# Optimization experiments

Hardware: AMD Instinct MI355X
Metric: run time of the kernel (lower is better)

Reference implementation:

```python
import jax, jax.numpy as jnp
import numpy as np

D_MODEL = 1024
N_HEADS = 16
D_K = D_MODEL // N_HEADS


def setup_inputs() -> dict:
    key = jax.random.key(0)
    kx, kq, kk, kv, ko = jax.random.split(key, 5)
    s = 1.0 / np.sqrt(D_MODEL)
    return {
        "x": jax.random.normal(kx, (4, 2048, D_MODEL), dtype=jnp.float32),
        "W_q": jax.random.normal(kq, (D_MODEL, D_MODEL), dtype=jnp.float32) * s,
        "W_k": jax.random.normal(kk, (D_MODEL, D_MODEL), dtype=jnp.float32) * s,
        "W_v": jax.random.normal(kv, (D_MODEL, D_MODEL), dtype=jnp.float32) * s,
        "W_o": jax.random.normal(ko, (D_MODEL, D_MODEL), dtype=jnp.float32) * s,
    }


def reference(x, W_q, W_k, W_v, W_o):
    B, S, _ = x.shape
    # torch nn.Linear computes x @ W.T; our W_* stored as [out, in]-equivalent square,
    # use plain x @ W (equivalent parameterization for a random weight).
    def split_heads(t):  # [B,S,D] -> [B,H,S,d_k]
        return t.reshape(B, S, N_HEADS, D_K).transpose(0, 2, 1, 3)

    Q = split_heads(x @ W_q)
    K = split_heads(x @ W_k)
    V = split_heads(x @ W_v)
    scale = 1.0 / np.sqrt(D_K).astype(np.float32)
    scores = jnp.einsum('bhqd,bhkd->bhqk', Q, K) * scale  # [B,H,S,S]
    causal_mask = jnp.tril(jnp.ones((S, S), dtype=bool))  # True = keep
    scores = jnp.where(causal_mask, scores, jnp.float32(-jnp.inf))
    attn = jax.nn.softmax(scores, axis=-1)
    out = jnp.einsum('bhqk,bhkd->bhqd', attn, V)  # [B,H,S,d_k]
    out = out.transpose(0, 2, 1, 3).reshape(B, S, D_MODEL)
    return out @ W_o
```

## Files before the change

kernel.cpp:

```cpp
#include <hip/hip_runtime.h>
#include <hip/hip_bf16.h>
#include <stdint.h>

#define B_SZ 4
#define SEQ 2048
#define DM 1024
#define NH 16
#define DK 64
#define BH (B_SZ * NH)
#define M_TOT (B_SZ * SEQ)

typedef unsigned short u16;
typedef u16 u16x8 __attribute__((ext_vector_type(8)));
typedef __bf16 bf16x8 __attribute__((ext_vector_type(8)));
typedef float f32x4 __attribute__((ext_vector_type(4)));

__device__ __forceinline__ u16 f2bf(float f) {
    union { float f; uint32_t u; } v; v.f = f;
    uint32_t u = v.u;
    return (u16)((u + 0x7FFFu + ((u >> 16) & 1u)) >> 16);
}

__device__ __forceinline__ u16 f2bf_trunc(float f) {
    union { float f; uint32_t u; } v; v.f = f;
    return (u16)(v.u >> 16);
}

__device__ __forceinline__ f32x4 mfma16(u16x8 a, u16x8 b, f32x4 c) {
    return __builtin_amdgcn_mfma_f32_16x16x32_bf16(
        __builtin_bit_cast(bf16x8, a), __builtin_bit_cast(bf16x8, b), c, 0, 0, 0);
}

__device__ __forceinline__ void gload16_lds(const void* g, void* l) {
    __builtin_amdgcn_global_load_lds(
        (const __attribute__((address_space(1))) void*)(uintptr_t)g,
        (__attribute__((address_space(3))) void*)(uintptr_t)l, 16, 0, 0);
}

__global__ void cvt_bf16_kernel(const float* __restrict__ in, u16* __restrict__ out, int n4) {
    int i = blockIdx.x * blockDim.x + threadIdx.x;
    if (i < n4) {
        float4 v = ((const float4*)in)[i];
        ushort4 o;
        o.x = f2bf(v.x); o.y = f2bf(v.y); o.z = f2bf(v.z); o.w = f2bf(v.w);
        ((ushort4*)out)[i] = o;
    }
}

__global__ void transpose_w_kernel(const float* __restrict__ W0, const float* __restrict__ W1,
                                   u16* __restrict__ Wt) {
    __shared__ u16 tile[32][33];
    int bx = blockIdx.x, by = blockIdx.y, z = blockIdx.z;
    const float* W = z ? W1 : W0;
    u16* Wd = Wt + (size_t)z * DM * DM;
    int t = threadIdx.x;
    for (int i = 0; i < 4; i++) {
        int idx = t + i * 256;
        int r = idx >> 5, c = idx & 31;
        tile[r][c] = f2bf(W[(by * 32 + r) * DM + bx * 32 + c]);
    }
    __syncthreads();
    for (int i = 0; i < 4; i++) {
        int idx = t + i * 256;
        int r2 = idx >> 5, c2 = idx & 31;
        Wd[(bx * 32 + r2) * DM + by * 32 + c2] = tile[c2][r2];
    }
}

__global__ void vtrans_kernel(const u16* __restrict__ V, u16* __restrict__ Vt) {
    __shared__ u16 t[64][66];
    int s0 = blockIdx.x * 64, bh = blockIdx.y;
    int tid = threadIdx.x, lane = tid & 63, wave = tid >> 6;
    const u16* Vg = V + (size_t)bh * SEQ * DK;
    u16* Og = Vt + (size_t)bh * DK * SEQ;
    for (int i = 0; i < 2; i++) {
        int s = lane;
        int dc = wave + 4 * i;
        u16x8 v = *(const u16x8*)(&Vg[(size_t)(s0 + s) * DK + dc * 8]);
        for (int j = 0; j < 8; j++) t[dc * 8 + j][s] = v[j];
    }
    __syncthreads();
    int d = tid >> 2, ch = tid & 3;
    u16 tmp[16];
    for (int j = 0; j < 16; j++) tmp[j] = t[d][ch * 16 + j];
    *(uint4*)(&Og[(size_t)d * SEQ + s0 + ch * 16]) = *(uint4*)(&tmp[0]);
    *(uint4*)(&Og[(size_t)d * SEQ + s0 + ch * 16 + 8]) = *(uint4*)(&tmp[8]);
}

template <int AFP32, int MODE>
__global__ __launch_bounds__(256, 2) void gemm128(
    const void* __restrict__ Ain, const u16* __restrict__ Bt,
    void* __restrict__ C0p, void* __restrict__ C1p, float scale0) {
    __shared__ u16 As[128][32];
    __shared__ u16 Bs[128][32];
    const int K = DM;
    int m0 = blockIdx.x * 128;
    int n0 = blockIdx.y * 128;
    int tid = threadIdx.x;
    int lane = tid & 63, wave = tid >> 6;
    int quad = lane >> 4, l15 = lane & 15;
    int wm = wave >> 1, wn = wave & 1;

    f32x4 acc[4][4];
    for (int i = 0; i < 4; i++)
        for (int j = 0; j < 4; j++) acc[i][j] = f32x4{0.f, 0.f, 0.f, 0.f};

    int rS = lane >> 2;
    int cS = (lane & 3) * 8;

    for (int k0 = 0; k0 < K; k0 += 32) {
        __syncthreads();
        if (AFP32) {
            const float* A = (const float*)Ain;
            for (int i = 0; i < 4; i++) {
                int idx = tid + i * 256;
                int r = idx >> 3, c = (idx & 7) * 4;
                float4 v = *(const float4*)(&A[(size_t)(m0 + r) * K + k0 + c]);
                ushort4 o;
                o.x = f2bf(v.x); o.y = f2bf(v.y); o.z = f2bf(v.z); o.w = f2bf(v.w);
                *(ushort4*)(&As[r][c]) = o;
            }
        } else {
            const u16* A = (const u16*)Ain;
            const u16* ga = &A[(size_t)(m0 + wave * 32 + rS) * K + k0 + cS];
            gload16_lds(ga, &As[wave * 32][0]);
            gload16_lds(ga + (size_t)16 * K, &As[wave * 32 + 16][0]);
        }
        {
            const u16* gb = &Bt[(size_t)(n0 + wave * 32 + rS) * K + k0 + cS];
            gload16_lds(gb, &Bs[wave * 32][0]);
            gload16_lds(gb + (size_t)16 * K, &Bs[wave * 32 + 16][0]);
        }
        __syncthreads();
        u16x8 af[4], bfv[4];
        for (int mt = 0; mt < 4; mt++)
            af[mt] = *(const u16x8*)(&As[wm * 64 + mt * 16 + l15][quad * 8]);
        for (int nt = 0; nt < 4; nt++)
            bfv[nt] = *(const u16x8*)(&Bs[wn * 64 + nt * 16 + l15][quad * 8]);
        for (int mt = 0; mt < 4; mt++)
            for (int nt = 0; nt < 4; nt++)
                acc[mt][nt] = mfma16(af[mt], bfv[nt], acc[mt][nt]);
    }

    for (int mt = 0; mt < 4; mt++)
        for (int nt = 0; nt < 4; nt++)
            for (int r = 0; r < 4; r++) {
                int m = m0 + wm * 64 + mt * 16 + quad * 4 + r;
                int n = n0 + wn * 64 + nt * 16 + l15;
                float v = acc[mt][nt][r];
                if (MODE == 0) {
                    v *= (n < 1024) ? scale0 : 1.0f;
                    u16* C = (n < 1024) ? (u16*)C0p : (u16*)C1p;
                    int ne = n & 1023;
                    int b = m >> 11, s = m & 2047;
                    int h = ne >> 6, d = ne & 63;
                    C[(((size_t)(b * NH + h) * SEQ) + s) * DK + d] = f2bf(v);
                } else {
                    ((float*)C0p)[(size_t)m * DM + n] = v;
                }
            }
}

__global__ __launch_bounds__(256, 4) void attn_kernel(
    const u16* __restrict__ Qb, const u16* __restrict__ Kb,
    const u16* __restrict__ Vtb, u16* __restrict__ AOb) {
    __shared__ u16 Kl[2][64][32];
    __shared__ u16 Vl[2][64][32];
    __shared__ u16 Pl[64][72];

    int bh = blockIdx.x;
    int p = blockIdx.y;
    int tid = threadIdx.x, lane = tid & 63, wave = tid >> 6;
    int quad = lane >> 4, l15 = lane & 15;
    int b = bh >> 4, h = bh & 15;

    const u16* Qg = Qb + (size_t)bh * SEQ * DK;
    const u16* Kg = Kb + (size_t)bh * SEQ * DK;
    const u16* Vg = Vtb + (size_t)bh * DK * SEQ;

    int rS = lane >> 2;
    int cS = (lane & 3) * 8;
    u16* Pw = &Pl[wave * 16][0];

    for (int ph = 0; ph < 2; ph++) {
        int qs = ph ? (31 - p) : p;
        int q0 = qs * 64;

        u16x8 aq[2];
        for (int kc = 0; kc < 2; kc++)
            aq[kc] = *(const u16x8*)(
                &Qg[(size_t)(q0 + wave * 16 + l15) * DK + kc * 32 + quad * 8]);

        float lsum[4];
        f32x4 O[4];
        for (int r = 0; r < 4; r++) lsum[r] = 0.f;
        for (int nt = 0; nt < 4; nt++) O[nt] = f32x4{0.f, 0.f, 0.f, 0.f};

        for (int kt = 0; kt <= qs; kt++) {
            int k0 = kt * 64;
            __syncthreads();
            {
                const u16* gk = &Kg[(size_t)(k0 + wave * 16 + rS) * DK + cS];
                gload16_lds(gk, &Kl[0][wave * 16][0]);
                gload16_lds(gk + 32, &Kl[1][wave * 16][0]);
                const u16* gv = &Vg[(size_t)(wave * 16 + rS) * SEQ + k0 + cS];
                gload16_lds(gv, &Vl[0][wave * 16][0]);
                gload16_lds(gv + 32, &Vl[1][wave * 16][0]);
            }
            __syncthreads();

            f32x4 sc[4];
            for (int nt = 0; nt < 4; nt++) {
                u16x8 b0 = *(const u16x8*)(&Kl[0][nt * 16 + l15][quad * 8]);
                u16x8 b1 = *(const u16x8*)(&Kl[1][nt * 16 + l15][quad * 8]);
                f32x4 z = f32x4{0.f, 0.f, 0.f, 0.f};
                z = mfma16(aq[0], b0, z);
                z = mfma16(aq[1], b1, z);
                sc[nt] = z;
            }
            if (kt == qs) {
                for (int nt = 0; nt < 4; nt++)
                    for (int r = 0; r < 4; r++) {
                        int qq = wave * 16 + quad * 4 + r;
                        int kk = nt * 16 + l15;
                        float e = exp2f(sc[nt][r]);
                        float pv = (kk <= qq) ? e : 0.f;
                        sc[nt][r] = pv;
                        lsum[r] += pv;
                    }
            } else {
                for (int nt = 0; nt < 4; nt++)
                    for (int r = 0; r < 4; r++) {
                        float pv = exp2f(sc[nt][r]);
                        sc[nt][r] = pv;
                        lsum[r] += pv;
                    }
            }
            for (int nt = 0; nt < 4; nt++)
                for (int r = 0; r < 4; r++)
                    Pw[(size_t)(quad * 4 + r) * 72 + nt * 16 + l15] = f2bf_trunc(sc[nt][r]);
            u16x8 ap0 = *(const u16x8*)(&Pw[(size_t)l15 * 72 + quad * 8]);
            u16x8 ap1 = *(const u16x8*)(&Pw[(size_t)l15 * 72 + 32 + quad * 8]);
            for (int nt = 0; nt < 4; nt++) {
                u16x8 b0 = *(const u16x8*)(&Vl[0][nt * 16 + l15][quad * 8]);
                u16x8 b1 = *(const u16x8*)(&Vl[1][nt * 16 + l15][quad * 8]);
                O[nt] = mfma16(ap0, b0, O[nt]);
                O[nt] = mfma16(ap1, b1, O[nt]);
            }
        }

        for (int r = 0; r < 4; r++) {
            float s = lsum[r];
            for (int off = 1; off < 16; off <<= 1) s += __shfl_xor(s, off, 64);
            float inv = 1.0f / s;
            int q = q0 + wave * 16 + quad * 4 + r;
            for (int nt = 0; nt < 4; nt++) {
                int d = nt * 16 + l15;
                AOb[((size_t)(b * SEQ + q)) * DM + h * DK + d] = f2bf(O[nt][r] * inv);
            }
        }
    }
}

extern "C" void kernel_launch(void* const* d_in, const int* in_sizes, int n_in,
                              void* d_out, int out_size, void* d_ws, size_t ws_size,
                              hipStream_t stream) {
    const float* x = (const float*)d_in[0];
    const float* Wq = (const float*)d_in[1];
    const float* Wk = (const float*)d_in[2];
    const float* Wv = (const float*)d_in[3];
    const float* Wo = (const float*)d_in[4];

    const size_t HALF = (size_t)M_TOT * DM * 2;
    char* S0 = (char*)d_ws;
    char* S1 = (char*)d_ws + HALF;
    char* D0 = (char*)d_out;
    char* D1 = (char*)d_out + HALF;

    u16* xb   = (u16*)S0;
    u16* Qb   = (u16*)S1;
    u16* Kb   = (u16*)D1;
    u16* Vb   = (u16*)D0;
    u16* Vt   = (u16*)S0;
    u16* AOb  = (u16*)D0;
    u16* wqk  = (u16*)D0;
    u16* wvt  = (u16*)S0;
    u16* wot  = (u16*)D1;
    float* Cf = (float*)d_ws;

    const float cscale = 0.125f * 1.44269504088896f;
    dim3 tg2(32, 32, 2);
    dim3 tg1(32, 32, 1);

    int n4 = M_TOT * DM / 4;
    cvt_bf16_kernel<<<n4 / 256, 256, 0, stream>>>(x, xb, n4);

    transpose_w_kernel<<<tg2, 256, 0, stream>>>(Wq, Wk, wqk);
    dim3 gqk(M_TOT / 128, 2048 / 128);
    gemm128<0, 0><<<gqk, 256, 0, stream>>>(xb, wqk, (void*)Qb, (void*)Kb, cscale);

    transpose_w_kernel<<<tg1, 256, 0, stream>>>(Wv, Wv, wvt);
    dim3 gg(M_TOT / 128, DM / 128);
    gemm128<1, 0><<<gg, 256, 0, stream>>>(x, wvt, (void*)Vb, (void*)Vb, 1.0f);

    dim3 vg(SEQ / 64, BH);
    vtrans_kernel<<<vg, 256, 0, stream>>>(Vb, Vt);

    dim3 ag(BH, 16);
    attn_kernel<<<ag, 256, 0, stream>>>(Qb, Kb, Vt, AOb);

    transpose_w_kernel<<<tg1, 256, 0, stream>>>(Wo, Wo, wot);
    gemm128<0, 1><<<gg, 256, 0, stream>>>(AOb, wot, (void*)Cf, (void*)Cf, 1.0f);

    hipMemcpyAsync(d_out, d_ws, 2 * HALF, hipMemcpyDeviceToDevice, stream);
}
```

Baseline: 296.8 us.

## Fuse V transpose into GEMM epilogue, split attention blocks, drop final memcpy

The V projection GEMM gets a new epilogue mode that writes the bf16 transposed V layout directly, which removes the separate transpose kernel and its read/write pass. The attention kernel no longer pairs a short and a long query tile per block. It launches one block per query tile with heaviest-first ordering and raises the occupancy hint to 6. The output projection now writes straight into the output buffer, so the final device-to-device memcpy is gone and buffer aliasing is rearranged. Risks are uncoalesced strided stores in the transposed epilogue and load imbalance without the paired tiles.

```diff
diff --git a/kernel.cpp b/kernel.cpp
--- a/kernel.cpp
+++ b/kernel.cpp
@@ -65,26 +65,6 @@
         int r2 = idx >> 5, c2 = idx & 31;
         Wd[(bx * 32 + r2) * DM + by * 32 + c2] = tile[c2][r2];
     }
-}
-
-__global__ void vtrans_kernel(const u16* __restrict__ V, u16* __restrict__ Vt) {
-    __shared__ u16 t[64][66];
-    int s0 = blockIdx.x * 64, bh = blockIdx.y;
-    int tid = threadIdx.x, lane = tid & 63, wave = tid >> 6;
-    const u16* Vg = V + (size_t)bh * SEQ * DK;
-    u16* Og = Vt + (size_t)bh * DK * SEQ;
-    for (int i = 0; i < 2; i++) {
-        int s = lane;
-        int dc = wave + 4 * i;
-        u16x8 v = *(const u16x8*)(&Vg[(size_t)(s0 + s) * DK + dc * 8]);
-        for (int j = 0; j < 8; j++) t[dc * 8 + j][s] = v[j];
-    }
-    __syncthreads();
-    int d = tid >> 2, ch = tid & 3;
-    u16 tmp[16];
-    for (int j = 0; j < 16; j++) tmp[j] = t[d][ch * 16 + j];
-    *(uint4*)(&Og[(size_t)d * SEQ + s0 + ch * 16]) = *(uint4*)(&tmp[0]);
-    *(uint4*)(&Og[(size_t)d * SEQ + s0 + ch * 16 + 8]) = *(uint4*)(&tmp[8]);
 }
 
 template <int AFP32, int MODE>
@@ -155,21 +135,26 @@
                     int b = m >> 11, s = m & 2047;
                     int h = ne >> 6, d = ne & 63;
                     C[(((size_t)(b * NH + h) * SEQ) + s) * DK + d] = f2bf(v);
+                } else if (MODE == 1) {
+                    ((float*)C0p)[(size_t)m * DM + n] = v;
                 } else {
-                    ((float*)C0p)[(size_t)m * DM + n] = v;
+                    int b = m >> 11, s = m & 2047;
+                    int h = n >> 6, d = n & 63;
+                    ((u16*)C0p)[(((size_t)(b * NH + h) * DK) + d) * SEQ + s] = f2bf(v);
                 }
             }
 }
 
-__global__ __launch_bounds__(256, 4) void attn_kernel(
+__global__ __launch_bounds__(256, 6) void attn_kernel(
     const u16* __restrict__ Qb, const u16* __restrict__ Kb,
     const u16* __restrict__ Vtb, u16* __restrict__ AOb) {
     __shared__ u16 Kl[2][64][32];
     __shared__ u16 Vl[2][64][32];
-    __shared__ u16 Pl[64][72];
+    __shared__ u16 Pl[64][68];
 
     int bh = blockIdx.x;
-    int p = blockIdx.y;
+    int qs = 31 - blockIdx.y;
+    int q0 = qs * 64;
     int tid = threadIdx.x, lane = tid & 63, wave = tid >> 6;
     int quad = lane >> 4, l15 = lane & 15;
     int b = bh >> 4, h = bh & 15;
@@ -182,82 +167,77 @@
     int cS = (lane & 3) * 8;
     u16* Pw = &Pl[wave * 16][0];
 
-    for (int ph = 0; ph < 2; ph++) {
-        int qs = ph ? (31 - p) : p;
-        int q0 = qs * 64;
-
-        u16x8 aq[2];
-        for (int kc = 0; kc < 2; kc++)
-            aq[kc] = *(const u16x8*)(
-                &Qg[(size_t)(q0 + wave * 16 + l15) * DK + kc * 32 + quad * 8]);
-
-        float lsum[4];
-        f32x4 O[4];
-        for (int r = 0; r < 4; r++) lsum[r] = 0.f;
-        for (int nt = 0; nt < 4; nt++) O[nt] = f32x4{0.f, 0.f, 0.f, 0.f};
-
-        for (int kt = 0; kt <= qs; kt++) {
-            int k0 = kt * 64;
-            __syncthreads();
-            {
-                const u16* gk = &Kg[(size_t)(k0 + wave * 16 + rS) * DK + cS];
-                gload16_lds(gk, &Kl[0][wave * 16][0]);
-                gload16_lds(gk + 32, &Kl[1][wave * 16][0]);
-                const u16* gv = &Vg[(size_t)(wave * 16 + rS) * SEQ + k0 + cS];
-                gload16_lds(gv, &Vl[0][wave * 16][0]);
-                gload16_lds(gv + 32, &Vl[1][wave * 16][0]);
-            }
-            __syncthreads();
-
-            f32x4 sc[4];
-            for (int nt = 0; nt < 4; nt++) {
-                u16x8 b0 = *(const u16x8*)(&Kl[0][nt * 16 + l15][quad * 8]);
-                u16x8 b1 = *(const u16x8*)(&Kl[1][nt * 16 + l15][quad * 8]);
-                f32x4 z = f32x4{0.f, 0.f, 0.f, 0.f};
-                z = mfma16(aq[0], b0, z);
-                z = mfma16(aq[1], b1, z);
-                sc[nt] = z;
-            }
-            if (kt == qs) {
-                for (int nt = 0; nt < 4; nt++)
-                    for (int r = 0; r < 4; r++) {
-                        int qq = wave * 16 + quad * 4 + r;
-                        int kk = nt * 16 + l15;
-                        float e = exp2f(sc[nt][r]);
-                        float pv = (kk <= qq) ? e : 0.f;
-                        sc[nt][r] = pv;
-                        lsum[r] += pv;
-                    }
-            } else {
-                for (int nt = 0; nt < 4; nt++)
-                    for (int r = 0; r < 4; r++) {
-                        float pv = exp2f(sc[nt][r]);
-                        sc[nt][r] = pv;
-                        lsum[r] += pv;
-                    }
-            }
+    u16x8 aq[2];
+    for (int kc = 0; kc < 2; kc++)
+        aq[kc] = *(const u16x8*)(
+            &Qg[(size_t)(q0 + wave * 16 + l15) * DK + kc * 32 + quad * 8]);
+
+    float lsum[4];
+    f32x4 O[4];
+    for (int r = 0; r < 4; r++) lsum[r] = 0.f;
+    for (int nt = 0; nt < 4; nt++) O[nt] = f32x4{0.f, 0.f, 0.f, 0.f};
+
+    for (int kt = 0; kt <= qs; kt++) {
+        int k0 = kt * 64;
+        __syncthreads();
+        {
+            const u16* gk = &Kg[(size_t)(k0 + wave * 16 + rS) * DK + cS];
+            gload16_lds(gk, &Kl[0][wave * 16][0]);
+            gload16_lds(gk + 32, &Kl[1][wave * 16][0]);
+            const u16* gv = &Vg[(size_t)(wave * 16 + rS) * SEQ + k0 + cS];
+            gload16_lds(gv, &Vl[0][wave * 16][0]);
+            gload16_lds(gv + 32, &Vl[1][wave * 16][0]);
+        }
+        __syncthreads();
+
+        f32x4 sc[4];
+        for (int nt = 0; nt < 4; nt++) {
+            u16x8 b0 = *(const u16x8*)(&Kl[0][nt * 16 + l15][quad * 8]);
+            u16x8 b1 = *(const u16x8*)(&Kl[1][nt * 16 + l15][quad * 8]);
+            f32x4 z = f32x4{0.f, 0.f, 0.f, 0.f};
+            z = mfma16(aq[0], b0, z);
+            z = mfma16(aq[1], b1, z);
+            sc[nt] = z;
+        }
+        if (kt == qs) {
             for (int nt = 0; nt < 4; nt++)
-                for (int r = 0; r < 4; r++)
-                    Pw[(size_t)(quad * 4 + r) * 72 + nt * 16 + l15] = f2bf_trunc(sc[nt][r]);
-            u16x8 ap0 = *(const u16x8*)(&Pw[(size_t)l15 * 72 + quad * 8]);
-            u16x8 ap1 = *(const u16x8*)(&Pw[(size_t)l15 * 72 + 32 + quad * 8]);
-            for (int nt = 0; nt < 4; nt++) {
-                u16x8 b0 = *(const u16x8*)(&Vl[0][nt * 16 + l15][quad * 8]);
-                u16x8 b1 = *(const u16x8*)(&Vl[1][nt * 16 + l15][quad * 8]);
-                O[nt] = mfma16(ap0, b0, O[nt]);
-                O[nt] = mfma16(ap1, b1, O[nt]);
-            }
-        }
-
-        for (int r = 0; r < 4; r++) {
-            float s = lsum[r];
-            for (int off = 1; off < 16; off <<= 1) s += __shfl_xor(s, off, 64);
-            float inv = 1.0f / s;
-            int q = q0 + wave * 16 + quad * 4 + r;
-            for (int nt = 0; nt < 4; nt++) {
-                int d = nt * 16 + l15;
-                AOb[((size_t)(b * SEQ + q)) * DM + h * DK + d] = f2bf(O[nt][r] * inv);
-            }
+                for (int r = 0; r < 4; r++) {
+                    int qq = wave * 16 + quad * 4 + r;
+                    int kk = nt * 16 + l15;
+                    float e = exp2f(sc[nt][r]);
+                    float pv = (kk <= qq) ? e : 0.f;
+                    sc[nt][r] = pv;
+                    lsum[r] += pv;
+                }
+        } else {
+            for (int nt = 0; nt < 4; nt++)
+                for (int r = 0; r < 4; r++) {
+                    float pv = exp2f(sc[nt][r]);
+                    sc[nt][r] = pv;
+                    lsum[r] += pv;
+                }
+        }
+        for (int nt = 0; nt < 4; nt++)
+            for (int r = 0; r < 4; r++)
+                Pw[(size_t)(quad * 4 + r) * 68 + nt * 16 + l15] = f2bf_trunc(sc[nt][r]);
+        u16x8 ap0 = *(const u16x8*)(&Pw[(size_t)l15 * 68 + quad * 8]);
+        u16x8 ap1 = *(const u16x8*)(&Pw[(size_t)l15 * 68 + 32 + quad * 8]);
+        for (int nt = 0; nt < 4; nt++) {
+            u16x8 b0 = *(const u16x8*)(&Vl[0][nt * 16 + l15][quad * 8]);
+            u16x8 b1 = *(const u16x8*)(&Vl[1][nt * 16 + l15][quad * 8]);
+            O[nt] = mfma16(ap0, b0, O[nt]);
+            O[nt] = mfma16(ap1, b1, O[nt]);
+        }
+    }
+
+    for (int r = 0; r < 4; r++) {
+        float s = lsum[r];
+        for (int off = 1; off < 16; off <<= 1) s += __shfl_xor(s, off, 64);
+        float inv = 1.0f / s;
+        int q = q0 + wave * 16 + quad * 4 + r;
+        for (int nt = 0; nt < 4; nt++) {
+            int d = nt * 16 + l15;
+            AOb[((size_t)(b * SEQ + q)) * DM + h * DK + d] = f2bf(O[nt][r] * inv);
         }
     }
 }
@@ -270,6 +250,7 @@
     const float* Wk = (const float*)d_in[2];
     const float* Wv = (const float*)d_in[3];
     const float* Wo = (const float*)d_in[4];
+    float* out = (float*)d_out;
 
     const size_t HALF = (size_t)M_TOT * DM * 2;
     char* S0 = (char*)d_ws;
@@ -277,20 +258,19 @@
     char* D0 = (char*)d_out;
     char* D1 = (char*)d_out + HALF;
 
-    u16* xb   = (u16*)S0;
-    u16* Qb   = (u16*)S1;
-    u16* Kb   = (u16*)D1;
-    u16* Vb   = (u16*)D0;
-    u16* Vt   = (u16*)S0;
-    u16* AOb  = (u16*)D0;
-    u16* wqk  = (u16*)D0;
-    u16* wvt  = (u16*)S0;
-    u16* wot  = (u16*)D1;
-    float* Cf = (float*)d_ws;
+    u16* xb  = (u16*)S0;
+    u16* Qb  = (u16*)S1;
+    u16* Kb  = (u16*)D1;
+    u16* Vt  = (u16*)D0;
+    u16* AOb = (u16*)S0;
+    u16* wqk = (u16*)D0;
+    u16* wvt = (u16*)S0;
+    u16* wot = (u16*)S1;
 
     const float cscale = 0.125f * 1.44269504088896f;
     dim3 tg2(32, 32, 2);
     dim3 tg1(32, 32, 1);
+    dim3 gg(M_TOT / 128, DM / 128);
 
     int n4 = M_TOT * DM / 4;
     cvt_bf16_kernel<<<n4 / 256, 256, 0, stream>>>(x, xb, n4);
@@ -300,17 +280,11 @@
     gemm128<0, 0><<<gqk, 256, 0, stream>>>(xb, wqk, (void*)Qb, (void*)Kb, cscale);
 
     transpose_w_kernel<<<tg1, 256, 0, stream>>>(Wv, Wv, wvt);
-    dim3 gg(M_TOT / 128, DM / 128);
-    gemm128<1, 0><<<gg, 256, 0, stream>>>(x, wvt, (void*)Vb, (void*)Vb, 1.0f);
-
-    dim3 vg(SEQ / 64, BH);
-    vtrans_kernel<<<vg, 256, 0, stream>>>(Vb, Vt);
-
-    dim3 ag(BH, 16);
+    gemm128<1, 2><<<gg, 256, 0, stream>>>(x, wvt, (void*)Vt, (void*)Vt, 1.0f);
+
+    dim3 ag(BH, 32);
     attn_kernel<<<ag, 256, 0, stream>>>(Qb, Kb, Vt, AOb);
 
     transpose_w_kernel<<<tg1, 256, 0, stream>>>(Wo, Wo, wot);
-    gemm128<0, 1><<<gg, 256, 0, stream>>>(AOb, wot, (void*)Cf, (void*)Cf, 1.0f);
-
-    hipMemcpyAsync(d_out, d_ws, 2 * HALF, hipMemcpyDeviceToDevice, stream);
-}
+    gemm128<0, 1><<<gg, 256, 0, stream>>>(AOb, wot, (void*)out, (void*)out, 1.0f);
+}
```

After: 296.6 us. About the same (-0.1%).
